# Performance work log

Measured on AMD Instinct MI355X. Metric: run time of the kernel, lower is better.

## Reference

```python
import jax, jax.numpy as jnp
import numpy as np

BS, CLS, C, H, W = 8, 4, 256, 128, 128
L, TK = 19, 256
MH, MW = 64, 64


def setup_inputs() -> dict:
    key = jax.random.key(0)
    ks = jax.random.split(key, 7)
    return {
        "mask_t": jax.random.uniform(ks[0], (BS, CLS, 1, MH, MW), dtype=jnp.float32),
        "fea_t": jax.random.normal(ks[1], (BS, C, H, W), dtype=jnp.float32),
        "token_s": jax.random.normal(ks[2], (BS, L, TK), dtype=jnp.float32),
        "W1": jax.random.normal(ks[3], (TK, C), dtype=jnp.float32) / np.sqrt(C),
        "W2": jax.random.normal(ks[4], (TK, TK), dtype=jnp.float32) / np.sqrt(TK),
        "W3": jax.random.normal(ks[5], (C, TK), dtype=jnp.float32) / np.sqrt(TK),
        "b3": jnp.zeros((C,), dtype=jnp.float32),
    }


def reference(mask_t, fea_t, token_s, W1, W2, W3, b3):
    bs, c, h, w = fea_t.shape
    cls = mask_t.shape[1]
    mh, mw = mask_t.shape[-2], mask_t.shape[-1]
    # F.interpolate nearest: out index i -> in index floor(i * in/out)
    ri = (jnp.arange(h) * mh) // h
    ci = (jnp.arange(w) * mw) // w
    m = mask_t.reshape(bs * cls, 1, mh, mw)[:, :, ri][:, :, :, ci]  # [bs*cls,1,h,w]
    # replicate torch's fea_t.repeat(cls,1,1,1) ordering (copy-major: index c*bs+b)
    # then the product is re-viewed batch-major (b*cls+c): fea index = (b*cls+cl) % bs
    idx = jnp.arange(bs * cls) % bs
    fea_c = (fea_t[idx] * m).reshape(bs, cls, c, h, w).mean(axis=1)  # [bs,c,h,w]
    q = fea_c.reshape(bs, c, h * w).transpose(0, 2, 1)  # [bs, HW, C]
    # forward_cell
    x_q = jnp.einsum('bnc,tc->bnt', q, W1)            # [bs,HW,TK]
    t_q = jnp.einsum('blc,tc->blt', token_s, W2)      # [bs,L,TK]
    a = jnp.einsum('bnt,blt->bnl', x_q, t_q)          # [bs,HW,L]
    a_soft = jax.nn.softmax(a / jnp.sqrt(jnp.float32(c)), axis=2)
    # sparse nonzero round-trip == zero out positions where logits are exactly 0
    a_soft = jnp.where(a != 0, a_soft, jnp.float32(0))
    t3 = jnp.einsum('blt,ot->blo', token_s, W3) + b3  # [bs,L,out]
    out = jnp.einsum('bnl,blo->bno', a_soft, t3)      # [bs,HW,out]
    out = out.transpose(0, 2, 1).reshape(bs, c, h, w)
    return out + fea_t
```

## Files before the change

### kernel.cpp

```cpp
#include <hip/hip_runtime.h>
#include <math.h>

#define BS   8
#define CLS  4
#define CCH  256
#define HH   128
#define WW   128
#define HWSZ (HH * WW)
#define LL   19
#define TKK  256
#define MHH  64
#define MWW  64

__global__ __launch_bounds__(256) void k_tok(
    const float* __restrict__ token, const float* __restrict__ W2,
    const float* __restrict__ W3, const float* __restrict__ b3,
    float* __restrict__ tq, float* __restrict__ t3g) {
  __shared__ float tok_s[TKK];
  const int bl = blockIdx.x;
  const int t  = threadIdx.x;
  tok_s[t] = token[bl * TKK + t];
  __syncthreads();
  const float4* w2r = (const float4*)(W2 + (size_t)t * TKK);
  const float4* w3r = (const float4*)(W3 + (size_t)t * TKK);
  float a2 = 0.f, a3 = 0.f;
#pragma unroll 8
  for (int i = 0; i < TKK / 4; ++i) {
    float4 x = w2r[i];
    float4 y = w3r[i];
    const float* ts = &tok_s[4 * i];
    a2 += x.x * ts[0] + x.y * ts[1] + x.z * ts[2] + x.w * ts[3];
    a3 += y.x * ts[0] + y.y * ts[1] + y.z * ts[2] + y.w * ts[3];
  }
  tq[bl * TKK + t]  = a2;
  t3g[bl * TKK + t] = a3 + b3[t];
}

__global__ __launch_bounds__(256) void k_u(
    const float* __restrict__ tq, const float* __restrict__ W1,
    float* __restrict__ u) {
  __shared__ float tq_s[TKK];
  const int bl = blockIdx.x;
  const int c  = threadIdx.x;
  tq_s[c] = tq[bl * TKK + c];
  __syncthreads();
  float a0 = 0.f, a1 = 0.f, a2 = 0.f, a3 = 0.f;
#pragma unroll 4
  for (int t = 0; t < TKK; t += 4) {
    a0 += W1[(t + 0) * CCH + c] * tq_s[t + 0];
    a1 += W1[(t + 1) * CCH + c] * tq_s[t + 1];
    a2 += W1[(t + 2) * CCH + c] * tq_s[t + 2];
    a3 += W1[(t + 3) * CCH + c] * tq_s[t + 3];
  }
  u[bl * CCH + c] = (a0 + a1 + a2 + a3) * (1.0f / 64.0f);
}

__global__ __launch_bounds__(256, 2) void k_main(
    const float* __restrict__ mask, const float* __restrict__ fea,
    const float* __restrict__ u, const float* __restrict__ t3g,
    float* __restrict__ out) {
  __shared__ float u_s[LL][CCH];
  __shared__ float t3_s[CCH * 20];
  __shared__ float part_s[4][LL][64];
  __shared__ float p_s[LL][64];

  const int blk  = blockIdx.x;
  const int b    = blk & 7;
  const int tile = blk >> 3;
  const int h    = tile >> 1;
  const int w0   = (tile & 1) << 6;
  const int n0   = h * WW + w0;
  const int t    = threadIdx.x;
  const int pix  = t & 63;
  const int wv   = t >> 6;

#pragma unroll
  for (int l = 0; l < LL; ++l) {
    u_s[l][t]       = u[(b * LL + l) * CCH + t];
    t3_s[t * 20 + l] = t3g[(b * LL + l) * CCH + t];
  }

  const int hrow = h >> 1;
  const int wcol = (w0 + pix) >> 1;
  float m0 = mask[(((size_t)(b * CLS + 0)) * MHH + hrow) * MWW + wcol];
  float m1 = mask[(((size_t)(b * CLS + 1)) * MHH + hrow) * MWW + wcol];
  float m2 = mask[(((size_t)(b * CLS + 2)) * MHH + hrow) * MWW + wcol];
  float m3 = mask[(((size_t)(b * CLS + 3)) * MHH + hrow) * MWW + wcol];

  __syncthreads();

  const int f0 = (b & 1) * 4;
  const float* fp0 = fea + ((size_t)(f0 + 0) * CCH) * HWSZ + n0 + pix;
  const float* fp1 = fea + ((size_t)(f0 + 1) * CCH) * HWSZ + n0 + pix;
  const float* fp2 = fea + ((size_t)(f0 + 2) * CCH) * HWSZ + n0 + pix;
  const float* fp3 = fea + ((size_t)(f0 + 3) * CCH) * HWSZ + n0 + pix;

  float facc[LL];
#pragma unroll
  for (int l = 0; l < LL; ++l) facc[l] = 0.f;

  const int c0 = wv * 64;
#pragma unroll 1
  for (int cc = 0; cc < 64; cc += 16) {
    float q[16];
#pragma unroll
    for (int j = 0; j < 16; ++j) {
      const size_t off = (size_t)(c0 + cc + j) * HWSZ;
      q[j] = fp0[off] * m0 + fp1[off] * m1 + fp2[off] * m2 + fp3[off] * m3;
    }
#pragma unroll
    for (int l = 0; l < LL; ++l) {
      const float4* ur = (const float4*)&u_s[l][c0 + cc];
      float s = facc[l];
#pragma unroll
      for (int jj = 0; jj < 4; ++jj) {
        const float4 uu = ur[jj];
        s += q[4 * jj + 0] * uu.x + q[4 * jj + 1] * uu.y +
             q[4 * jj + 2] * uu.z + q[4 * jj + 3] * uu.w;
      }
      facc[l] = s;
    }
  }

#pragma unroll
  for (int l = 0; l < LL; ++l) part_s[wv][l][pix] = facc[l];
  __syncthreads();

  if (t < 64) {
    float a[LL];
    float mx = -INFINITY;
#pragma unroll
    for (int l = 0; l < LL; ++l) {
      a[l] = part_s[0][l][t] + part_s[1][l][t] + part_s[2][l][t] + part_s[3][l][t];
      mx = fmaxf(mx, a[l]);
    }
    float e[LL];
    float sum = 0.f;
#pragma unroll
    for (int l = 0; l < LL; ++l) { e[l] = __expf(a[l] - mx); sum += e[l]; }
    const float inv = 1.0f / sum;
#pragma unroll
    for (int l = 0; l < LL; ++l)
      p_s[l][t] = (a[l] != 0.f) ? e[l] * inv : 0.f;
  }
  __syncthreads();

  float p[LL];
#pragma unroll
  for (int l = 0; l < LL; ++l) p[l] = p_s[l][pix];

  const int ob = wv * 64;
#pragma unroll 2
  for (int i = 0; i < 64; ++i) {
    const int o = ob + i;
    const float4* tr = (const float4*)&t3_s[o * 20];
    float tv[20];
#pragma unroll
    for (int jj = 0; jj < 5; ++jj) {
      const float4 x = tr[jj];
      tv[4 * jj + 0] = x.x; tv[4 * jj + 1] = x.y;
      tv[4 * jj + 2] = x.z; tv[4 * jj + 3] = x.w;
    }
    float s = 0.f;
#pragma unroll
    for (int l = 0; l < LL; ++l) s += p[l] * tv[l];
    const size_t off = ((size_t)(b * CCH + o)) * HWSZ + n0 + pix;
    out[off] = s + fea[off];
  }
}

extern "C" void kernel_launch(void* const* d_in, const int* in_sizes, int n_in,
                              void* d_out, int out_size, void* d_ws, size_t ws_size,
                              hipStream_t stream) {
  (void)in_sizes; (void)n_in; (void)out_size; (void)ws_size;
  const float* mask  = (const float*)d_in[0];
  const float* fea   = (const float*)d_in[1];
  const float* token = (const float*)d_in[2];
  const float* W1    = (const float*)d_in[3];
  const float* W2    = (const float*)d_in[4];
  const float* W3    = (const float*)d_in[5];
  const float* b3    = (const float*)d_in[6];
  float* out = (float*)d_out;

  float* tq = (float*)d_ws;
  float* u  = tq + BS * LL * TKK;
  float* t3 = u + BS * LL * CCH;

  k_tok<<<BS * LL, 256, 0, stream>>>(token, W2, W3, b3, tq, t3);
  k_u<<<BS * LL, 256, 0, stream>>>(tq, W1, u);
  k_main<<<(HWSZ / 64) * BS, 256, 0, stream>>>(mask, fea, u, t3, out);
}
```

Before: 392.7 us.

## Fuse token prep kernels and widen main tile to full rows with float2

Merges the two small token-projection kernels into one, which also writes t3 pre-transposed with stride 20. The main kernel now covers a full 128-pixel row per block, with each lane handling two pixels through float2 loads. The cross-wave reduction now goes through shared-memory atomics, and t3 is read from global/L2 with wave-uniform addressing instead of being staged in LDS. Launch bounds rise to 4 blocks per SM. The goal is fewer launches, less LDS and more occupancy, at the cost of smaller channel chunks per iteration and LDS atomic contention.

```diff
diff --git a/kernel.cpp b/kernel.cpp
--- a/kernel.cpp
+++ b/kernel.cpp
@@ -12,14 +12,18 @@
 #define MHH  64
 #define MWW  64
 
-__global__ __launch_bounds__(256) void k_tok(
-    const float* __restrict__ token, const float* __restrict__ W2,
-    const float* __restrict__ W3, const float* __restrict__ b3,
-    float* __restrict__ tq, float* __restrict__ t3g) {
+__global__ __launch_bounds__(256) void k_prep(
+    const float* __restrict__ token, const float* __restrict__ W1,
+    const float* __restrict__ W2, const float* __restrict__ W3,
+    const float* __restrict__ b3, float* __restrict__ u,
+    float* __restrict__ t3t) {
   __shared__ float tok_s[TKK];
+  __shared__ float tq_s[TKK];
   const int bl = blockIdx.x;
+  const int b  = bl / LL;
+  const int l  = bl - b * LL;
   const int t  = threadIdx.x;
-  tok_s[t] = token[bl * TKK + t];
+  tok_s[t] = token[(size_t)bl * TKK + t];
   __syncthreads();
   const float4* w2r = (const float4*)(W2 + (size_t)t * TKK);
   const float4* w3r = (const float4*)(W3 + (size_t)t * TKK);
@@ -32,108 +36,91 @@
     a2 += x.x * ts[0] + x.y * ts[1] + x.z * ts[2] + x.w * ts[3];
     a3 += y.x * ts[0] + y.y * ts[1] + y.z * ts[2] + y.w * ts[3];
   }
-  tq[bl * TKK + t]  = a2;
-  t3g[bl * TKK + t] = a3 + b3[t];
+  tq_s[t] = a2;
+  t3t[((size_t)b * CCH + t) * 20 + l] = a3 + b3[t];
+  __syncthreads();
+  float s0 = 0.f, s1 = 0.f, s2 = 0.f, s3 = 0.f;
+#pragma unroll 4
+  for (int k = 0; k < TKK; k += 4) {
+    s0 += W1[(k + 0) * CCH + t] * tq_s[k + 0];
+    s1 += W1[(k + 1) * CCH + t] * tq_s[k + 1];
+    s2 += W1[(k + 2) * CCH + t] * tq_s[k + 2];
+    s3 += W1[(k + 3) * CCH + t] * tq_s[k + 3];
+  }
+  u[(size_t)bl * CCH + t] = (s0 + s1 + s2 + s3) * (1.0f / 64.0f);
 }
 
-__global__ __launch_bounds__(256) void k_u(
-    const float* __restrict__ tq, const float* __restrict__ W1,
-    float* __restrict__ u) {
-  __shared__ float tq_s[TKK];
-  const int bl = blockIdx.x;
-  const int c  = threadIdx.x;
-  tq_s[c] = tq[bl * TKK + c];
-  __syncthreads();
-  float a0 = 0.f, a1 = 0.f, a2 = 0.f, a3 = 0.f;
-#pragma unroll 4
-  for (int t = 0; t < TKK; t += 4) {
-    a0 += W1[(t + 0) * CCH + c] * tq_s[t + 0];
-    a1 += W1[(t + 1) * CCH + c] * tq_s[t + 1];
-    a2 += W1[(t + 2) * CCH + c] * tq_s[t + 2];
-    a3 += W1[(t + 3) * CCH + c] * tq_s[t + 3];
-  }
-  u[bl * CCH + c] = (a0 + a1 + a2 + a3) * (1.0f / 64.0f);
-}
-
-__global__ __launch_bounds__(256, 2) void k_main(
+__global__ __launch_bounds__(256, 4) void k_main(
     const float* __restrict__ mask, const float* __restrict__ fea,
-    const float* __restrict__ u, const float* __restrict__ t3g,
+    const float* __restrict__ u, const float* __restrict__ t3t,
     float* __restrict__ out) {
   __shared__ float u_s[LL][CCH];
-  __shared__ float t3_s[CCH * 20];
-  __shared__ float part_s[4][LL][64];
-  __shared__ float p_s[LL][64];
+  __shared__ float acc_s[LL][128];
 
   const int blk  = blockIdx.x;
   const int b    = blk & 7;
   const int tile = blk >> 3;
-  const int h    = tile >> 1;
-  const int w0   = (tile & 1) << 6;
-  const int n0   = h * WW + w0;
+  const int n0   = tile * WW;
   const int t    = threadIdx.x;
-  const int pix  = t & 63;
+  const int lane = t & 63;
   const int wv   = t >> 6;
 
 #pragma unroll
-  for (int l = 0; l < LL; ++l) {
-    u_s[l][t]       = u[(b * LL + l) * CCH + t];
-    t3_s[t * 20 + l] = t3g[(b * LL + l) * CCH + t];
-  }
+  for (int l = 0; l < LL; ++l) u_s[l][t] = u[((size_t)b * LL + l) * CCH + t];
+  for (int k = t; k < LL * 128; k += 256) ((float*)acc_s)[k] = 0.f;
 
-  const int hrow = h >> 1;
-  const int wcol = (w0 + pix) >> 1;
-  float m0 = mask[(((size_t)(b * CLS + 0)) * MHH + hrow) * MWW + wcol];
-  float m1 = mask[(((size_t)(b * CLS + 1)) * MHH + hrow) * MWW + wcol];
-  float m2 = mask[(((size_t)(b * CLS + 2)) * MHH + hrow) * MWW + wcol];
-  float m3 = mask[(((size_t)(b * CLS + 3)) * MHH + hrow) * MWW + wcol];
+  const int hrow = tile >> 1;
+  const float m0 = mask[(((size_t)(b * CLS + 0)) * MHH + hrow) * MWW + lane];
+  const float m1 = mask[(((size_t)(b * CLS + 1)) * MHH + hrow) * MWW + lane];
+  const float m2 = mask[(((size_t)(b * CLS + 2)) * MHH + hrow) * MWW + lane];
+  const float m3 = mask[(((size_t)(b * CLS + 3)) * MHH + hrow) * MWW + lane];
 
   __syncthreads();
 
   const int f0 = (b & 1) * 4;
-  const float* fp0 = fea + ((size_t)(f0 + 0) * CCH) * HWSZ + n0 + pix;
-  const float* fp1 = fea + ((size_t)(f0 + 1) * CCH) * HWSZ + n0 + pix;
-  const float* fp2 = fea + ((size_t)(f0 + 2) * CCH) * HWSZ + n0 + pix;
-  const float* fp3 = fea + ((size_t)(f0 + 3) * CCH) * HWSZ + n0 + pix;
+  const float* fb0 = fea + (size_t)(f0 + 0) * CCH * HWSZ + n0;
+  const float* fb1 = fea + (size_t)(f0 + 1) * CCH * HWSZ + n0;
+  const float* fb2 = fea + (size_t)(f0 + 2) * CCH * HWSZ + n0;
+  const float* fb3 = fea + (size_t)(f0 + 3) * CCH * HWSZ + n0;
 
-  float facc[LL];
+  float facc[LL][2];
 #pragma unroll
-  for (int l = 0; l < LL; ++l) facc[l] = 0.f;
+  for (int l = 0; l < LL; ++l) { facc[l][0] = 0.f; facc[l][1] = 0.f; }
 
   const int c0 = wv * 64;
 #pragma unroll 1
-  for (int cc = 0; cc < 64; cc += 16) {
-    float q[16];
+  for (int cc = 0; cc < 64; cc += 4) {
+    float2 q[4];
 #pragma unroll
-    for (int j = 0; j < 16; ++j) {
-      const size_t off = (size_t)(c0 + cc + j) * HWSZ;
-      q[j] = fp0[off] * m0 + fp1[off] * m1 + fp2[off] * m2 + fp3[off] * m3;
+    for (int j = 0; j < 4; ++j) {
+      const size_t coff = (size_t)(c0 + cc + j) * HWSZ;
+      const float2 v0 = ((const float2*)(fb0 + coff))[lane];
+      const float2 v1 = ((const float2*)(fb1 + coff))[lane];
+      const float2 v2 = ((const float2*)(fb2 + coff))[lane];
+      const float2 v3 = ((const float2*)(fb3 + coff))[lane];
+      q[j].x = v0.x * m0 + v1.x * m1 + v2.x * m2 + v3.x * m3;
+      q[j].y = v0.y * m0 + v1.y * m1 + v2.y * m2 + v3.y * m3;
     }
 #pragma unroll
     for (int l = 0; l < LL; ++l) {
-      const float4* ur = (const float4*)&u_s[l][c0 + cc];
-      float s = facc[l];
-#pragma unroll
-      for (int jj = 0; jj < 4; ++jj) {
-        const float4 uu = ur[jj];
-        s += q[4 * jj + 0] * uu.x + q[4 * jj + 1] * uu.y +
-             q[4 * jj + 2] * uu.z + q[4 * jj + 3] * uu.w;
-      }
-      facc[l] = s;
+      const float4 uu = *(const float4*)&u_s[l][c0 + cc];
+      facc[l][0] += q[0].x * uu.x + q[1].x * uu.y + q[2].x * uu.z + q[3].x * uu.w;
+      facc[l][1] += q[0].y * uu.x + q[1].y * uu.y + q[2].y * uu.z + q[3].y * uu.w;
     }
   }
 
 #pragma unroll
-  for (int l = 0; l < LL; ++l) part_s[wv][l][pix] = facc[l];
+  for (int l = 0; l < LL; ++l) {
+    atomicAdd(&acc_s[l][2 * lane + 0], facc[l][0]);
+    atomicAdd(&acc_s[l][2 * lane + 1], facc[l][1]);
+  }
   __syncthreads();
 
-  if (t < 64) {
+  if (t < 128) {
     float a[LL];
     float mx = -INFINITY;
 #pragma unroll
-    for (int l = 0; l < LL; ++l) {
-      a[l] = part_s[0][l][t] + part_s[1][l][t] + part_s[2][l][t] + part_s[3][l][t];
-      mx = fmaxf(mx, a[l]);
-    }
+    for (int l = 0; l < LL; ++l) { a[l] = acc_s[l][t]; mx = fmaxf(mx, a[l]); }
     float e[LL];
     float sum = 0.f;
 #pragma unroll
@@ -141,31 +128,33 @@
     const float inv = 1.0f / sum;
 #pragma unroll
     for (int l = 0; l < LL; ++l)
-      p_s[l][t] = (a[l] != 0.f) ? e[l] * inv : 0.f;
+      acc_s[l][t] = (a[l] != 0.f) ? e[l] * inv : 0.f;
   }
   __syncthreads();
 
-  float p[LL];
+  float2 p[LL];
 #pragma unroll
-  for (int l = 0; l < LL; ++l) p[l] = p_s[l][pix];
+  for (int l = 0; l < LL; ++l) p[l] = *(const float2*)&acc_s[l][2 * lane];
 
-  const int ob = wv * 64;
+  const int wvu = __builtin_amdgcn_readfirstlane(wv);
+  const int ob  = wvu * 64;
 #pragma unroll 2
   for (int i = 0; i < 64; ++i) {
     const int o = ob + i;
-    const float4* tr = (const float4*)&t3_s[o * 20];
-    float tv[20];
+    const float* tr = t3t + ((size_t)b * CCH + o) * 20;
+    float sx = 0.f, sy = 0.f;
 #pragma unroll
-    for (int jj = 0; jj < 5; ++jj) {
-      const float4 x = tr[jj];
-      tv[4 * jj + 0] = x.x; tv[4 * jj + 1] = x.y;
-      tv[4 * jj + 2] = x.z; tv[4 * jj + 3] = x.w;
+    for (int l = 0; l < LL; ++l) {
+      const float tv = tr[l];
+      sx += p[l].x * tv;
+      sy += p[l].y * tv;
     }
-    float s = 0.f;
-#pragma unroll
-    for (int l = 0; l < LL; ++l) s += p[l] * tv[l];
-    const size_t off = ((size_t)(b * CCH + o)) * HWSZ + n0 + pix;
-    out[off] = s + fea[off];
+    const size_t off = ((size_t)b * CCH + o) * HWSZ + n0;
+    const float2 r = ((const float2*)(fea + off))[lane];
+    float2 res;
+    res.x = sx + r.x;
+    res.y = sy + r.y;
+    ((float2*)(out + off))[lane] = res;
   }
 }
 
@@ -182,11 +171,9 @@
   const float* b3    = (const float*)d_in[6];
   float* out = (float*)d_out;
 
-  float* tq = (float*)d_ws;
-  float* u  = tq + BS * LL * TKK;
-  float* t3 = u + BS * LL * CCH;
+  float* u   = (float*)d_ws;
+  float* t3t = u + BS * LL * CCH;
 
-  k_tok<<<BS * LL, 256, 0, stream>>>(token, W2, W3, b3, tq, t3);
-  k_u<<<BS * LL, 256, 0, stream>>>(tq, W1, u);
-  k_main<<<(HWSZ / 64) * BS, 256, 0, stream>>>(mask, fea, u, t3, out);
+  k_prep<<<BS * LL, 256, 0, stream>>>(token, W1, W2, W3, b3, u, t3t);
+  k_main<<<(HWSZ / WW) * BS, 256, 0, stream>>>(mask, fea, u, t3t, out);
 }
```

After: 393.7 us. Within noise of the previous version (+0.3%).
